# Performance work log

Hardware: AMD Instinct MI355X
Metric: run time of the kernel (lower is better)

## Reference

```python
import jax, jax.numpy as jnp
import numpy as np

HEAD_DIM = 64
N_HEADS = 32
N_KV_HEADS = 8
ROPE_THETA = 10000.0


def _rotate_half(x):
    h = x.shape[-1] // 2
    return jnp.concatenate([-x[..., h:], x[..., :h]], axis=-1)


def _rope_cos_sin(position_ids, head_dim, theta, dtype):
    # position_ids: [b, s] int
    inv_freq = 1.0 / (theta ** (jnp.arange(0, head_dim, 2, dtype=jnp.float32) / head_dim))
    freqs = position_ids.astype(jnp.float32)[..., None] * inv_freq  # [b, s, hd/2]
    emb = jnp.concatenate([freqs, freqs], axis=-1)                  # [b, s, hd]
    return jnp.cos(emb).astype(dtype), jnp.sin(emb).astype(dtype)


def setup_inputs() -> dict:
    key = jax.random.key(0)
    ks = jax.random.split(key, 5)
    B, S, H = 2, 2048, 2048
    KVD = N_KV_HEADS * HEAD_DIM
    x = jax.random.normal(ks[0], (B, S, H), dtype=jnp.float32)
    position_ids = jnp.broadcast_to(jnp.arange(S, dtype=jnp.int64), (B, S))
    # additive causal mask: 0 on/below diagonal, -1e9 above
    causal = jnp.triu(jnp.full((S, S), -1e9, dtype=jnp.float32), k=1)
    mask = causal[None, None, :, :]
    sc = 1.0 / np.sqrt(H)
    wq = jax.random.normal(ks[1], (H, H), dtype=jnp.float32) * sc
    wk = jax.random.normal(ks[2], (KVD, H), dtype=jnp.float32) * sc
    wv = jax.random.normal(ks[3], (KVD, H), dtype=jnp.float32) * sc
    wo = jax.random.normal(ks[4], (H, H), dtype=jnp.float32) * sc
    return {"x": x, "position_ids": position_ids, "mask": mask,
            "wq": wq, "wk": wk, "wv": wv, "wo": wo}


def reference(x, position_ids, mask, wq, wk, wv, wo):
    b, s, h = x.shape
    kv_groups = N_HEADS // N_KV_HEADS
    # projections (Linear with weight [out, in])
    xq = jnp.einsum('bsh,oh->bso', x, wq)
    xk = jnp.einsum('bsh,oh->bso', x, wk)
    xv = jnp.einsum('bsh,oh->bso', x, wv)
    q = xq.reshape(b, s, N_HEADS, HEAD_DIM).transpose(0, 2, 1, 3)      # [b,H,s,d]
    k = xk.reshape(b, s, N_KV_HEADS, HEAD_DIM).transpose(0, 2, 1, 3)   # [b,Hk,s,d]
    v = xv.reshape(b, s, N_KV_HEADS, HEAD_DIM).transpose(0, 2, 1, 3)
    cos, sin = _rope_cos_sin(position_ids, HEAD_DIM, ROPE_THETA, x.dtype)
    cos = cos[:, None, :, :]  # [b,1,s,d]
    sin = sin[:, None, :, :]
    q = q * cos + _rotate_half(q) * sin
    k = k * cos + _rotate_half(k) * sin
    # GQA expand
    k = jnp.repeat(k, kv_groups, axis=1)  # [b,H,s,d]
    v = jnp.repeat(v, kv_groups, axis=1)
    scale = 1.0 / np.sqrt(HEAD_DIM)
    attn = jnp.einsum('bhqd,bhkd->bhqk', q, k) * scale
    attn = attn + mask[:, :, :s, :s]
    attn = jax.nn.softmax(attn.astype(jnp.float32), axis=-1).astype(q.dtype)
    out = jnp.einsum('bhqk,bhkd->bhqd', attn, v)        # [b,H,s,d]
    out = out.transpose(0, 2, 1, 3).reshape(b, s, h)
    return jnp.einsum('bsh,oh->bso', out, wo)
```

## Files before the change

kernel.cpp:

```cpp
#include <hip/hip_runtime.h>

typedef __bf16 bf16;
typedef __bf16 bf16x4 __attribute__((ext_vector_type(4)));
typedef __bf16 bf16x8 __attribute__((ext_vector_type(8)));
typedef float f32x4 __attribute__((ext_vector_type(4)));

#define MFMA16(a, b, c) __builtin_amdgcn_mfma_f32_16x16x32_bf16(a, b, c, 0, 0, 0)
#define L2E 1.44269504088896340736f

__device__ inline float exp2_hw(float x) {
  float r;
  asm("v_exp_f32 %0, %1" : "=v"(r) : "v"(x));
  return r;
}

__device__ inline bf16x8 cvt8(const float* __restrict__ p) {
  float4 f0 = ((const float4*)p)[0];
  float4 f1 = ((const float4*)p)[1];
  bf16x8 v;
  v[0] = (bf16)f0.x; v[1] = (bf16)f0.y; v[2] = (bf16)f0.z; v[3] = (bf16)f0.w;
  v[4] = (bf16)f1.x; v[5] = (bf16)f1.y; v[6] = (bf16)f1.z; v[7] = (bf16)f1.w;
  return v;
}

__device__ inline void gl_lds16(const bf16* g, bf16* l) {
  __builtin_amdgcn_global_load_lds(
      (const __attribute__((address_space(1))) unsigned int*)g,
      (__attribute__((address_space(3))) unsigned int*)l, 16, 0, 0);
}

__global__ void detect_kernel(const unsigned* __restrict__ mask,
                              int* __restrict__ flag) {
  *flag = (mask[0] != 0u) ? 1 : 0;
}

__global__ __launch_bounds__(256) void convert_kernel(
    const void* __restrict__ s0, bf16* __restrict__ d0, int n0,
    const void* __restrict__ s1, bf16* __restrict__ d1, int n1,
    const void* __restrict__ s2, bf16* __restrict__ d2, int n2,
    const void* __restrict__ s3, bf16* __restrict__ d3, int n3,
    float2* __restrict__ tab, const int* __restrict__ flag) {
  const int gid = blockIdx.x * 256 + threadIdx.x;
  if (tab && gid < 65536) {
    int s = gid >> 5, fi = gid & 31;
    float inv = 1.0f / powf(10000.0f, (float)(2 * fi) / 64.0f);
    float fr = (float)s * inv;
    tab[gid] = make_float2(cosf(fr), sinf(fr));
  }
  const int isb = *flag;
  const int c0 = n0 >> 3, c1 = c0 + (n1 >> 3), c2 = c1 + (n2 >> 3);
  const int total = c2 + (n3 >> 3);
  for (int c = gid; c < total; c += gridDim.x * 256) {
    const void* s; bf16* d; int off;
    if (c < c0)      { s = s0; d = d0; off = c; }
    else if (c < c1) { s = s1; d = d1; off = c - c0; }
    else if (c < c2) { s = s2; d = d2; off = c - c1; }
    else             { s = s3; d = d3; off = c - c2; }
    if (isb) ((uint4*)d)[off] = ((const uint4*)s)[off];
    else     ((bf16x8*)d)[off] = cvt8((const float*)s + (size_t)off * 8);
  }
}

template <int MODE>
__global__ __launch_bounds__(256) void gemm_bt(
    const bf16* __restrict__ Ab, const bf16* __restrict__ Wq,
    const bf16* __restrict__ Wk, const bf16* __restrict__ Wv,
    void* __restrict__ O0, bf16* __restrict__ O1, bf16* __restrict__ O2,
    const float2* __restrict__ rtab, const int* __restrict__ flag) {
  const int K = 2048;
  __shared__ __align__(16) bf16 As[128 * 32];
  __shared__ __align__(16) bf16 Bs[128 * 32];

  const int m0 = blockIdx.x * 128;
  const int n0 = blockIdx.y * 128;

  const bf16* W;
  int nw0;
  if (MODE == 0) {
    if (n0 < 2048) { W = Wq; nw0 = n0; }
    else if (n0 < 2560) { W = Wk; nw0 = n0 - 2048; }
    else { W = Wv; nw0 = n0 - 2560; }
  } else {
    W = Wq; nw0 = n0;
  }

  const int t = threadIdx.x;
  const int w = t >> 6, lane = t & 63, quad = lane >> 4, l15 = lane & 15;
  const int wm = (w >> 1) * 64, wn = (w & 1) * 64;

  const int ca = t, cb = t + 256;
  const bf16* ga0 = Ab + (size_t)(m0 + (ca >> 2)) * K + (ca & 3) * 8;
  const bf16* ga1 = Ab + (size_t)(m0 + (cb >> 2)) * K + (cb & 3) * 8;
  const bf16* gb0 = W + (size_t)(nw0 + (ca >> 2)) * K + (ca & 3) * 8;
  const bf16* gb1 = W + (size_t)(nw0 + (cb >> 2)) * K + (cb & 3) * 8;
  bf16* lA0 = &As[w * 512];
  bf16* lA1 = &As[2048 + w * 512];
  bf16* lB0 = &Bs[w * 512];
  bf16* lB1 = &Bs[2048 + w * 512];

  f32x4 acc[4][4] = {};

  for (int k0 = 0; k0 < K; k0 += 32) {
    __syncthreads();
    gl_lds16(ga0 + k0, lA0);
    gl_lds16(ga1 + k0, lA1);
    gl_lds16(gb0 + k0, lB0);
    gl_lds16(gb1 + k0, lB1);
    __syncthreads();

    bf16x8 a[4], b[4];
#pragma unroll
    for (int i = 0; i < 4; i++)
      a[i] = *(const bf16x8*)&As[(wm + i * 16 + l15) * 32 + quad * 8];
#pragma unroll
    for (int j = 0; j < 4; j++)
      b[j] = *(const bf16x8*)&Bs[(wn + j * 16 + l15) * 32 + quad * 8];
#pragma unroll
    for (int i = 0; i < 4; i++)
#pragma unroll
      for (int j = 0; j < 4; j++)
        acc[i][j] = MFMA16(a[i], b[j], acc[i][j]);
  }

  if (MODE == 0 && n0 >= 2560) {
#pragma unroll
    for (int i = 0; i < 4; i++)
#pragma unroll
      for (int j = 0; j < 4; j++) {
        int m = m0 + wm + i * 16 + quad * 4;
        int n = (n0 - 2560) + wn + j * 16 + l15;
        int hh = n >> 6, d = n & 63;
        int b_ = m >> 11, s = m & 2047;
        bf16x4 pv;
#pragma unroll
        for (int r = 0; r < 4; r++) pv[r] = (bf16)acc[i][j][r];
        *(bf16x4*)&O2[(((size_t)b_ * 8 + hh) * 64 + d) * 2048 + s] = pv;
      }
    return;
  }

  const int isb = *flag;

  if (MODE == 0) {
#pragma unroll
    for (int i = 0; i < 4; i++) {
      int mb = m0 + wm + i * 16 + quad * 4;
#pragma unroll
      for (int r = 0; r < 4; r++) {
        int s = (mb + r) & 2047;
#pragma unroll
        for (int jp = 0; jp < 2; jp++) {
          int fi = jp * 16 + l15;
          float2 cs = rtab[s * 32 + fi];
          float cb = cs.x, sb = cs.y;
          if (isb) { cb = (float)(bf16)cb; sb = (float)(bf16)sb; }
          float v0 = acc[i][jp][r], v1 = acc[i][jp + 2][r];
          acc[i][jp][r]     = v0 * cb - v1 * sb;
          acc[i][jp + 2][r] = v1 * cb + v0 * sb;
        }
      }
    }
    const bool isQ = (n0 < 2048);
    const float qs = isQ ? 0.125f : 1.0f;
#pragma unroll
    for (int i = 0; i < 4; i++)
#pragma unroll
      for (int j = 0; j < 4; j++)
#pragma unroll
        for (int r = 0; r < 4; r++) {
          int m = m0 + wm + i * 16 + quad * 4 + r;
          int b_ = m >> 11, s = m & 2047;
          bf16 bv = (bf16)(acc[i][j][r] * qs);
          if (isQ) {
            int n = n0 + wn + j * 16 + l15;
            int h = n >> 6, d = n & 63;
            ((bf16*)O0)[(((size_t)b_ * 32 + h) * 2048 + s) * 64 + d] = bv;
          } else {
            int nn = n0 - 2048 + wn + j * 16 + l15;
            int h = nn >> 6, d = nn & 63;
            O1[(((size_t)b_ * 8 + h) * 2048 + s) * 64 + d] = bv;
          }
        }
    return;
  }

#pragma unroll
  for (int i = 0; i < 4; i++)
#pragma unroll
    for (int j = 0; j < 4; j++)
#pragma unroll
      for (int r = 0; r < 4; r++) {
        int m = m0 + wm + i * 16 + quad * 4 + r;
        int n = n0 + wn + j * 16 + l15;
        float fv = acc[i][j][r];
        if (isb) ((bf16*)O0)[(size_t)m * 2048 + n] = (bf16)fv;
        else     ((float*)O0)[(size_t)m * 2048 + n] = fv;
      }
}

__global__ __launch_bounds__(512) void flash_kernel(
    const bf16* __restrict__ qb, const bf16* __restrict__ kb,
    const bf16* __restrict__ vb, bf16* __restrict__ ao) {
  __shared__ __align__(16) bf16 SM[8704 + 8 * 16 * 72];
  bf16* Ks = SM;
  bf16* Vt = SM + 4096;
  bf16* Ps = SM + 8704;

  const int bx = blockIdx.x;
  const int h = blockIdx.y;
  const int b = blockIdx.z;
  const int kvh = h >> 2;
  const int t = threadIdx.x, w = t >> 6, lane = t & 63;
  const int quad = lane >> 4, l15 = lane & 15;

  const bf16* kg = kb + ((size_t)b * 8 + kvh) * 2048 * 64;
  const bf16* vg = vb + ((size_t)b * 8 + kvh) * 64 * 2048;

  const int srow = t >> 3;
  const int sslot = t & 7;
  const int kofs = srow * 64 + ((sslot ^ (srow & 7)) << 3);
  const int vofs = srow * 72 + sslot * 8;
  bf16* psw = Ps + w * (16 * 72);

#pragma unroll 1
  for (int ti = 0; ti < 2; ti++) {
    const int tile = (ti == 0) ? bx : 15 - bx;
    const int q0b = tile * 128;
    const bf16* qg = qb + (((size_t)b * 32 + h) * 2048 + q0b) * 64;

    __syncthreads();
#pragma unroll
    for (int i = 0; i < 2; i++) {
      int c = t + i * 512;
      int row = c >> 3, slot = c & 7;
      *(uint4*)&SM[row * 64 + ((slot ^ (row & 7)) << 3)] = ((const uint4*)qg)[c];
    }
    uint4 kr = ((const uint4*)kg)[t];
    uint4 vr = *(const uint4*)(vg + (size_t)srow * 2048 + sslot * 8);
    __syncthreads();
    const int qrow = w * 16 + l15;
    bf16x8 aq0 = *(const bf16x8*)&SM[qrow * 64 + ((quad ^ (qrow & 7)) << 3)];
    bf16x8 aq1 = *(const bf16x8*)&SM[qrow * 64 + (((4 + quad) ^ (qrow & 7)) << 3)];

    f32x4 Oacc[4] = {};
    float m_sm = -1e30f, l_sm = 0.0f;

    const int nk = q0b + 128;
    const int qmin = q0b + w * 16;
    const int qmax = qmin + 15;
    const int qr_sm = qmin + l15;

    for (int k0 = 0; k0 < nk; k0 += 64) {
      __syncthreads();
      *(uint4*)&Ks[kofs] = kr;
      *(uint4*)&Vt[vofs] = vr;
      __syncthreads();

      if (k0 + 64 < nk) {
        kr = *((const uint4*)(kg + (size_t)(k0 + 64) * 64) + t);
        vr = *(const uint4*)(vg + (size_t)srow * 2048 + (k0 + 64) + sslot * 8);
      }

      f32x4 sf[4] = {};
#pragma unroll
      for (int sub = 0; sub < 4; sub++) {
        if (k0 + sub * 16 <= qmax) {
          int rr = sub * 16 + l15;
          bf16x8 bk0 = *(const bf16x8*)&Ks[rr * 64 + ((quad ^ (rr & 7)) << 3)];
          bf16x8 bk1 = *(const bf16x8*)&Ks[rr * 64 + (((4 + quad) ^ (rr & 7)) << 3)];
          sf[sub] = MFMA16(bk0, aq0, sf[sub]);
          sf[sub] = MFMA16(bk1, aq1, sf[sub]);
        }
      }

      if (k0 + 64 > qmin) {
#pragma unroll
        for (int sub = 0; sub < 4; sub++) {
          int kk = k0 + sub * 16 + quad * 4;
#pragma unroll
          for (int r = 0; r < 4; r++)
            if (kk + r > qr_sm) sf[sub][r] = -1e30f;
        }
      }

      float mx;
      {
        f32x4 t4;
#pragma unroll
        for (int r = 0; r < 4; r++)
          t4[r] = fmaxf(fmaxf(sf[0][r], sf[1][r]), fmaxf(sf[2][r], sf[3][r]));
        mx = fmaxf(fmaxf(t4[0], t4[1]), fmaxf(t4[2], t4[3]));
      }
      mx = fmaxf(mx, __shfl_xor(mx, 16));
      mx = fmaxf(mx, __shfl_xor(mx, 32));

      if (!__all(mx <= m_sm + 8.0f)) {
        float mnew = fmaxf(m_sm, mx);
        float alpha = exp2_hw((m_sm - mnew) * L2E);
        l_sm *= alpha;
        m_sm = mnew;
        f32x4 apv;
#pragma unroll
        for (int r = 0; r < 4; r++) apv[r] = __shfl(alpha, quad * 4 + r);
#pragma unroll
        for (int tt = 0; tt < 4; tt++)
#pragma unroll
          for (int r = 0; r < 4; r++) Oacc[tt][r] *= apv[r];
      }

      const float ml2 = m_sm * L2E;
#pragma unroll
      for (int sub = 0; sub < 4; sub++)
#pragma unroll
        for (int r = 0; r < 4; r++)
          sf[sub][r] = exp2_hw(fmaf(sf[sub][r], L2E, -ml2));

      float rs;
      {
        f32x4 t4;
#pragma unroll
        for (int r = 0; r < 4; r++)
          t4[r] = (sf[0][r] + sf[1][r]) + (sf[2][r] + sf[3][r]);
        rs = (t4[0] + t4[1]) + (t4[2] + t4[3]);
      }
      rs += __shfl_xor(rs, 16);
      rs += __shfl_xor(rs, 32);
      l_sm += rs;

#pragma unroll
      for (int sub = 0; sub < 4; sub++) {
        bf16x4 pk;
#pragma unroll
        for (int r = 0; r < 4; r++) pk[r] = (bf16)sf[sub][r];
        *(bf16x4*)&psw[l15 * 72 + sub * 16 + quad * 4] = pk;
      }
      asm volatile("s_waitcnt lgkmcnt(0)" ::: "memory");
      __builtin_amdgcn_sched_barrier(0);

      bf16x8 ap0 = *(const bf16x8*)&psw[l15 * 72 + quad * 8];
#pragma unroll
      for (int tt = 0; tt < 4; tt++) {
        bf16x8 bv = *(const bf16x8*)&Vt[(tt * 16 + l15) * 72 + quad * 8];
        Oacc[tt] = MFMA16(ap0, bv, Oacc[tt]);
      }
      if (k0 + 32 <= qmax) {
        bf16x8 ap1 = *(const bf16x8*)&psw[l15 * 72 + 32 + quad * 8];
#pragma unroll
        for (int tt = 0; tt < 4; tt++) {
          bf16x8 bv = *(const bf16x8*)&Vt[(tt * 16 + l15) * 72 + 32 + quad * 8];
          Oacc[tt] = MFMA16(ap1, bv, Oacc[tt]);
        }
      }
    }

    f32x4 lv;
#pragma unroll
    for (int r = 0; r < 4; r++) lv[r] = __shfl(l_sm, quad * 4 + r);
#pragma unroll
    for (int tt = 0; tt < 4; tt++)
#pragma unroll
      for (int r = 0; r < 4; r++) {
        int m = q0b + w * 16 + quad * 4 + r;
        ao[((size_t)b * 2048 + m) * 2048 + h * 64 + tt * 16 + l15] =
            (bf16)(Oacc[tt][r] / lv[r]);
      }
  }
}

extern "C" void kernel_launch(void* const* d_in, const int* in_sizes, int n_in,
                              void* d_out, int out_size, void* d_ws,
                              size_t ws_size, hipStream_t stream) {
  const void* x = d_in[0];
  const unsigned* maskw = (const unsigned*)d_in[2];
  const void* wq = d_in[3];
  const void* wk = d_in[4];
  const void* wv = d_in[5];
  const void* wo = d_in[6];

  char* ws = (char*)d_ws;
  bf16* qbuf  = (bf16*)(ws);
  bf16* kbuf  = (bf16*)(ws + 16777216);
  bf16* vbuf  = (bf16*)(ws + 20971520);
  bf16* wob   = (bf16*)(ws + 16777216);
  bf16* aobuf = (bf16*)(ws + 25165824);
  bf16* xb    = (bf16*)(ws + 25165824);
  int* flag   = (int*)(ws + 41943040);
  bf16* wqb   = (bf16*)(ws + 41943104);
  bf16* wkb   = (bf16*)(ws + 50331712);
  bf16* wvb   = (bf16*)(ws + 52428864);
  float2* rtab = (float2*)(ws + 54526016);

  detect_kernel<<<1, 1, 0, stream>>>(maskw, flag);
  convert_kernel<<<2048, 256, 0, stream>>>(x, xb, 8388608, wq, wqb, 4194304,
                                           wk, wkb, 1048576, wv, wvb, 1048576,
                                           rtab, flag);
  gemm_bt<0><<<dim3(32, 24), 256, 0, stream>>>(xb, wqb, wkb, wvb, qbuf, kbuf,
                                               vbuf, rtab, flag);
  flash_kernel<<<dim3(8, 32, 2), 512, 0, stream>>>(qbuf, kbuf, vbuf, aobuf);
  convert_kernel<<<2048, 256, 0, stream>>>(wo, wob, 4194304, nullptr, nullptr,
                                           0, nullptr, nullptr, 0, nullptr,
                                           nullptr, 0, nullptr, flag);
  gemm_bt<1><<<dim3(32, 16), 256, 0, stream>>>(aobuf, wob, nullptr, nullptr,
                                               d_out, nullptr, nullptr, rtab,
                                               flag);
}
```

Baseline: 352.1 us.

## Shrink GEMM N-tile to 64 and XOR-swizzle LDS tiles against bank conflicts

The projection GEMMs move from 128x128 to 128x64 output tiles, so each wave now computes a 32x64 sub-tile and the grids double to 32x48 and 32x16→32x32. Global-to-LDS loads now permute the four 16-byte K-chunks of each row with an XOR of row bits, and the fragment reads apply the same permutation, to cut LDS bank conflicts. The goal is better CU fill and fewer LDS stalls. The cost is less operand reuse per block and more total global traffic for the A matrix.

```diff
diff --git a/kernel.cpp b/kernel.cpp
--- a/kernel.cpp
+++ b/kernel.cpp
@@ -69,10 +69,10 @@
     const float2* __restrict__ rtab, const int* __restrict__ flag) {
   const int K = 2048;
   __shared__ __align__(16) bf16 As[128 * 32];
-  __shared__ __align__(16) bf16 Bs[128 * 32];
+  __shared__ __align__(16) bf16 Bs[64 * 32];
 
   const int m0 = blockIdx.x * 128;
-  const int n0 = blockIdx.y * 128;
+  const int n0 = blockIdx.y * 64;
 
   const bf16* W;
   int nw0;
@@ -86,37 +86,36 @@
 
   const int t = threadIdx.x;
   const int w = t >> 6, lane = t & 63, quad = lane >> 4, l15 = lane & 15;
-  const int wm = (w >> 1) * 64, wn = (w & 1) * 64;
 
   const int ca = t, cb = t + 256;
-  const bf16* ga0 = Ab + (size_t)(m0 + (ca >> 2)) * K + (ca & 3) * 8;
-  const bf16* ga1 = Ab + (size_t)(m0 + (cb >> 2)) * K + (cb & 3) * 8;
-  const bf16* gb0 = W + (size_t)(nw0 + (ca >> 2)) * K + (ca & 3) * 8;
-  const bf16* gb1 = W + (size_t)(nw0 + (cb >> 2)) * K + (cb & 3) * 8;
+  const int ra = ca >> 2, rb = cb >> 2;
+  const bf16* ga0 = Ab + (size_t)(m0 + ra) * K + (((ca & 3) ^ ((ra >> 1) & 3)) * 8);
+  const bf16* ga1 = Ab + (size_t)(m0 + rb) * K + (((cb & 3) ^ ((rb >> 1) & 3)) * 8);
+  const bf16* gb0 = W + (size_t)(nw0 + ra) * K + (((ca & 3) ^ ((ra >> 1) & 3)) * 8);
   bf16* lA0 = &As[w * 512];
   bf16* lA1 = &As[2048 + w * 512];
   bf16* lB0 = &Bs[w * 512];
-  bf16* lB1 = &Bs[2048 + w * 512];
-
-  f32x4 acc[4][4] = {};
+
+  f32x4 acc[2][4] = {};
+
+  const int sa = (quad ^ ((l15 >> 1) & 3)) << 3;
 
   for (int k0 = 0; k0 < K; k0 += 32) {
     __syncthreads();
     gl_lds16(ga0 + k0, lA0);
     gl_lds16(ga1 + k0, lA1);
     gl_lds16(gb0 + k0, lB0);
-    gl_lds16(gb1 + k0, lB1);
     __syncthreads();
 
-    bf16x8 a[4], b[4];
-#pragma unroll
-    for (int i = 0; i < 4; i++)
-      a[i] = *(const bf16x8*)&As[(wm + i * 16 + l15) * 32 + quad * 8];
+    bf16x8 a[2], b[4];
+#pragma unroll
+    for (int i = 0; i < 2; i++)
+      a[i] = *(const bf16x8*)&As[(w * 32 + i * 16 + l15) * 32 + sa];
 #pragma unroll
     for (int j = 0; j < 4; j++)
-      b[j] = *(const bf16x8*)&Bs[(wn + j * 16 + l15) * 32 + quad * 8];
-#pragma unroll
-    for (int i = 0; i < 4; i++)
+      b[j] = *(const bf16x8*)&Bs[(j * 16 + l15) * 32 + sa];
+#pragma unroll
+    for (int i = 0; i < 2; i++)
 #pragma unroll
       for (int j = 0; j < 4; j++)
         acc[i][j] = MFMA16(a[i], b[j], acc[i][j]);
@@ -124,11 +123,11 @@
 
   if (MODE == 0 && n0 >= 2560) {
 #pragma unroll
-    for (int i = 0; i < 4; i++)
+    for (int i = 0; i < 2; i++)
 #pragma unroll
       for (int j = 0; j < 4; j++) {
-        int m = m0 + wm + i * 16 + quad * 4;
-        int n = (n0 - 2560) + wn + j * 16 + l15;
+        int m = m0 + w * 32 + i * 16 + quad * 4;
+        int n = (n0 - 2560) + j * 16 + l15;
         int hh = n >> 6, d = n & 63;
         int b_ = m >> 11, s = m & 2047;
         bf16x4 pv;
@@ -143,8 +142,8 @@
 
   if (MODE == 0) {
 #pragma unroll
-    for (int i = 0; i < 4; i++) {
-      int mb = m0 + wm + i * 16 + quad * 4;
+    for (int i = 0; i < 2; i++) {
+      int mb = m0 + w * 32 + i * 16 + quad * 4;
 #pragma unroll
       for (int r = 0; r < 4; r++) {
         int s = (mb + r) & 2047;
@@ -163,20 +162,20 @@
     const bool isQ = (n0 < 2048);
     const float qs = isQ ? 0.125f : 1.0f;
 #pragma unroll
-    for (int i = 0; i < 4; i++)
+    for (int i = 0; i < 2; i++)
 #pragma unroll
       for (int j = 0; j < 4; j++)
 #pragma unroll
         for (int r = 0; r < 4; r++) {
-          int m = m0 + wm + i * 16 + quad * 4 + r;
+          int m = m0 + w * 32 + i * 16 + quad * 4 + r;
           int b_ = m >> 11, s = m & 2047;
           bf16 bv = (bf16)(acc[i][j][r] * qs);
           if (isQ) {
-            int n = n0 + wn + j * 16 + l15;
+            int n = n0 + j * 16 + l15;
             int h = n >> 6, d = n & 63;
             ((bf16*)O0)[(((size_t)b_ * 32 + h) * 2048 + s) * 64 + d] = bv;
           } else {
-            int nn = n0 - 2048 + wn + j * 16 + l15;
+            int nn = n0 - 2048 + j * 16 + l15;
             int h = nn >> 6, d = nn & 63;
             O1[(((size_t)b_ * 8 + h) * 2048 + s) * 64 + d] = bv;
           }
@@ -185,13 +184,13 @@
   }
 
 #pragma unroll
-  for (int i = 0; i < 4; i++)
+  for (int i = 0; i < 2; i++)
 #pragma unroll
     for (int j = 0; j < 4; j++)
 #pragma unroll
       for (int r = 0; r < 4; r++) {
-        int m = m0 + wm + i * 16 + quad * 4 + r;
-        int n = n0 + wn + j * 16 + l15;
+        int m = m0 + w * 32 + i * 16 + quad * 4 + r;
+        int n = n0 + j * 16 + l15;
         float fv = acc[i][j][r];
         if (isb) ((bf16*)O0)[(size_t)m * 2048 + n] = (bf16)fv;
         else     ((float*)O0)[(size_t)m * 2048 + n] = fv;
@@ -394,13 +393,13 @@
   convert_kernel<<<2048, 256, 0, stream>>>(x, xb, 8388608, wq, wqb, 4194304,
                                            wk, wkb, 1048576, wv, wvb, 1048576,
                                            rtab, flag);
-  gemm_bt<0><<<dim3(32, 24), 256, 0, stream>>>(xb, wqb, wkb, wvb, qbuf, kbuf,
+  gemm_bt<0><<<dim3(32, 48), 256, 0, stream>>>(xb, wqb, wkb, wvb, qbuf, kbuf,
                                                vbuf, rtab, flag);
   flash_kernel<<<dim3(8, 32, 2), 512, 0, stream>>>(qbuf, kbuf, vbuf, aobuf);
   convert_kernel<<<2048, 256, 0, stream>>>(wo, wob, 4194304, nullptr, nullptr,
                                            0, nullptr, nullptr, 0, nullptr,
                                            nullptr, 0, nullptr, flag);
-  gemm_bt<1><<<dim3(32, 16), 256, 0, stream>>>(aobuf, wob, nullptr, nullptr,
+  gemm_bt<1><<<dim3(32, 32), 256, 0, stream>>>(aobuf, wob, nullptr, nullptr,
                                                d_out, nullptr, nullptr, rtab,
                                                flag);
 }
```

Result: faster. 340.4 us (-3.3%).

## Double-buffer GEMM LDS tiles with async prefetch and XOR-swizzled layout

Applied to the files above, without the earlier changes.

The projection GEMM now keeps two LDS buffers per operand and issues the global-to-LDS loads for the next K tile before computing on the current one, using vmcnt waits and raw barriers in place of two __syncthreads per iteration. The LDS columns are also XOR-swizzled by row, through the global source offsets and the fragment reads, to cut bank conflicts on the bf16x8 reads. This aims to hide global load latency behind MFMA work, at the cost of doubled LDS use, which may lower occupancy, and fragile hand-written waitcnt logic.

```diff
diff --git a/kernel.cpp b/kernel.cpp
--- a/kernel.cpp
+++ b/kernel.cpp
@@ -68,8 +68,8 @@
     void* __restrict__ O0, bf16* __restrict__ O1, bf16* __restrict__ O2,
     const float2* __restrict__ rtab, const int* __restrict__ flag) {
   const int K = 2048;
-  __shared__ __align__(16) bf16 As[128 * 32];
-  __shared__ __align__(16) bf16 Bs[128 * 32];
+  __shared__ __align__(16) bf16 As[2][128 * 32];
+  __shared__ __align__(16) bf16 Bs[2][128 * 32];
 
   const int m0 = blockIdx.x * 128;
   const int n0 = blockIdx.y * 128;
@@ -89,37 +89,55 @@
   const int wm = (w >> 1) * 64, wn = (w & 1) * 64;
 
   const int ca = t, cb = t + 256;
-  const bf16* ga0 = Ab + (size_t)(m0 + (ca >> 2)) * K + (ca & 3) * 8;
-  const bf16* ga1 = Ab + (size_t)(m0 + (cb >> 2)) * K + (cb & 3) * 8;
-  const bf16* gb0 = W + (size_t)(nw0 + (ca >> 2)) * K + (ca & 3) * 8;
-  const bf16* gb1 = W + (size_t)(nw0 + (cb >> 2)) * K + (cb & 3) * 8;
-  bf16* lA0 = &As[w * 512];
-  bf16* lA1 = &As[2048 + w * 512];
-  bf16* lB0 = &Bs[w * 512];
-  bf16* lB1 = &Bs[2048 + w * 512];
+  const int ra = ca >> 2, rb = cb >> 2;
+  const int sga = ((ca & 3) ^ ((ra >> 1) & 3)) * 8;
+  const int sgb = ((cb & 3) ^ ((rb >> 1) & 3)) * 8;
+  const bf16* ga0 = Ab + (size_t)(m0 + ra) * K + sga;
+  const bf16* ga1 = Ab + (size_t)(m0 + rb) * K + sgb;
+  const bf16* gb0 = W + (size_t)(nw0 + ra) * K + sga;
+  const bf16* gb1 = W + (size_t)(nw0 + rb) * K + sgb;
 
   f32x4 acc[4][4] = {};
 
-  for (int k0 = 0; k0 < K; k0 += 32) {
-    __syncthreads();
-    gl_lds16(ga0 + k0, lA0);
-    gl_lds16(ga1 + k0, lA1);
-    gl_lds16(gb0 + k0, lB0);
-    gl_lds16(gb1 + k0, lB1);
-    __syncthreads();
+  const int sa = (quad ^ ((l15 >> 1) & 3)) << 3;
+
+  const int NT = K / 32;
+  gl_lds16(ga0, &As[0][w * 512]);
+  gl_lds16(ga1, &As[0][2048 + w * 512]);
+  gl_lds16(gb0, &Bs[0][w * 512]);
+  gl_lds16(gb1, &Bs[0][2048 + w * 512]);
+
+#pragma unroll 2
+  for (int ti = 0; ti < NT; ti++) {
+    const int cur = ti & 1;
+    const int k0 = ti * 32;
+    if (ti + 1 < NT) {
+      const int nxt = cur ^ 1;
+      gl_lds16(ga0 + k0 + 32, &As[nxt][w * 512]);
+      gl_lds16(ga1 + k0 + 32, &As[nxt][2048 + w * 512]);
+      gl_lds16(gb0 + k0 + 32, &Bs[nxt][w * 512]);
+      gl_lds16(gb1 + k0 + 32, &Bs[nxt][2048 + w * 512]);
+      asm volatile("s_waitcnt vmcnt(4)" ::: "memory");
+    } else {
+      asm volatile("s_waitcnt vmcnt(0)" ::: "memory");
+    }
+    __builtin_amdgcn_s_barrier();
 
     bf16x8 a[4], b[4];
 #pragma unroll
     for (int i = 0; i < 4; i++)
-      a[i] = *(const bf16x8*)&As[(wm + i * 16 + l15) * 32 + quad * 8];
+      a[i] = *(const bf16x8*)&As[cur][(wm + i * 16 + l15) * 32 + sa];
 #pragma unroll
     for (int j = 0; j < 4; j++)
-      b[j] = *(const bf16x8*)&Bs[(wn + j * 16 + l15) * 32 + quad * 8];
+      b[j] = *(const bf16x8*)&Bs[cur][(wn + j * 16 + l15) * 32 + sa];
 #pragma unroll
     for (int i = 0; i < 4; i++)
 #pragma unroll
       for (int j = 0; j < 4; j++)
         acc[i][j] = MFMA16(a[i], b[j], acc[i][j]);
+
+    asm volatile("s_waitcnt lgkmcnt(0)" ::: "memory");
+    __builtin_amdgcn_s_barrier();
   }
 
   if (MODE == 0 && n0 >= 2560) {
```

Result: no change. 353.7 us (+0.4%).
